# Kernel optimization log

Hardware: AMD Instinct MI355X
Metric: run time of the kernel (lower is better)

Reference implementation:

```python
import jax, jax.numpy as jnp
import numpy as np

B, N = 4, 2048
VD, CD = 256, 64
H = 4
INNER = VD  # inner_ratio = 1
D = INNER // H  # head_dim = 64
EPS = 1e-5
RMS_EPS = 1e-6


def layer_norm(x, g, b):
    m = jnp.mean(x, axis=-1, keepdims=True)
    v = jnp.mean((x - m) ** 2, axis=-1, keepdims=True)
    return (x - m) * jax.lax.rsqrt(v + EPS) * g + b


def rms_norm(x, s):
    ms = jnp.mean(x * x, axis=-1, keepdims=True)
    return x * jax.lax.rsqrt(ms + RMS_EPS) * s


def split_heads(x):  # (b, n, h*d) -> (b, h, n, d)
    b, n, _ = x.shape
    return x.reshape(b, n, H, D).transpose(0, 2, 1, 3)


def setup_inputs() -> dict:
    key = jax.random.key(0)
    ks = jax.random.split(key, 10)
    w = lambda k, shp: jax.random.normal(k, shp, dtype=jnp.float32) * 0.02
    return {
        "V": jax.random.normal(ks[0], (B, N, VD), dtype=jnp.float32),
        "C": jax.random.normal(ks[1], (B, N, CD), dtype=jnp.float32),
        "vn_g": jnp.ones((VD,), jnp.float32), "vn_b": jnp.zeros((VD,), jnp.float32),
        "cn_g": jnp.ones((CD,), jnp.float32), "cn_b": jnp.zeros((CD,), jnp.float32),
        "W_vqk": w(ks[2], (VD, 2 * INNER)), "b_vqk": jnp.zeros((2 * INNER,), jnp.float32),
        "rms_v": jnp.ones((2 * INNER,), jnp.float32),
        "W_cqk": w(ks[3], (CD, 2 * INNER)), "b_cqk": jnp.zeros((2 * INNER,), jnp.float32),
        "rms_c": jnp.ones((2 * INNER,), jnp.float32),
        "W_vv": w(ks[4], (VD, INNER)), "b_vv": jnp.zeros((INNER,), jnp.float32),
        "W_cv": w(ks[5], (CD, INNER)), "b_cv": jnp.zeros((INNER,), jnp.float32),
        "W_ov": w(ks[6], (INNER, VD)), "b_ov": jnp.zeros((VD,), jnp.float32),
        "W_oc": w(ks[7], (INNER, CD)), "b_oc": jnp.zeros((CD,), jnp.float32),
    }


def reference(V, C, vn_g, vn_b, cn_g, cn_b, W_vqk, b_vqk, rms_v, W_cqk, b_cqk, rms_c,
              W_vv, b_vv, W_cv, b_cv, W_ov, b_ov, W_oc, b_oc):
    Vn = layer_norm(V, vn_g, vn_b)
    Cn = layer_norm(C, cn_g, cn_b)
    qkv = rms_norm(Vn @ W_vqk + b_vqk, rms_v)
    qkc = rms_norm(Cn @ W_cqk + b_cqk, rms_c)
    qv, kv = jnp.split(qkv, 2, axis=-1)
    qc, kc = jnp.split(qkc, 2, axis=-1)
    vv = Vn @ W_vv + b_vv
    vc = Cn @ W_cv + b_cv
    qv, kv, vv, qc, kc, vc = map(split_heads, (qv, kv, vv, qc, kc, vc))
    # shared attention map: softmax((QvKv^T + QcKc^T)/sqrt(d))
    scores = (jnp.einsum("bhnd,bhmd->bhnm", qv, kv)
              + jnp.einsum("bhnd,bhmd->bhnm", qc, kc)) / np.sqrt(D).astype(np.float32)
    attn = jax.nn.softmax(scores, axis=-1)
    out_v = jnp.einsum("bhnm,bhmd->bhnd", attn, vv).transpose(0, 2, 1, 3).reshape(B, N, INNER)
    out_c = jnp.einsum("bhnm,bhmd->bhnd", attn, vc).transpose(0, 2, 1, 3).reshape(B, N, INNER)
    return out_v @ W_ov + b_ov, out_c @ W_oc + b_oc
```

## Files before the change

### kernel.cpp

```cpp
#include <hip/hip_runtime.h>

typedef unsigned short u16;
typedef unsigned int   u32;
typedef short s16x8 __attribute__((ext_vector_type(8)));
typedef float f32x4 __attribute__((ext_vector_type(4)));

#define WS_STATSV 0
#define WS_STATSC 65536
#define WS_WT_VQK 131072
#define WS_WT_CQK 393216
#define WS_WT_VV  458752
#define WS_WT_CV  589824
#define WS_WT_OV  622592
#define WS_WT_OC  753664
#define WS_Q      786432
#define WS_K      9175040
#define WS_VT     17563648
#define WS_OV     25952256
#define WS_OC     30146560

__device__ __forceinline__ float bf2f(u16 h){
  union { u32 u; float f; } x; x.u = ((u32)h) << 16; return x.f;
}
__device__ __forceinline__ u16 f2bf(float f){
  union { float f; u32 u; } x; x.f = f;
  u32 u = x.u; u += 0x7fffu + ((u >> 16) & 1u);
  return (u16)(u >> 16);
}
__device__ __forceinline__ f32x4 mfma16(s16x8 a, s16x8 b, f32x4 c){
  return __builtin_amdgcn_mfma_f32_16x16x32_bf16(a, b, c, 0, 0, 0);
}

__global__ __launch_bounds__(256) void k_prep(const float* V, const float* C,
    const float* vng, const float* vnb, const float* cng, const float* cnb,
    const float* Wvqk, const float* Wcqk, const float* Wvv, const float* Wcv,
    const float* Wov, const float* Woc, char* ws){
  int bid = blockIdx.x;
  if (bid < 4096){
    int wid = threadIdx.x >> 6, lane = threadIdx.x & 63;
    if (bid < 2048){
      int row = bid*4 + wid;
      const float4* p = (const float4*)(V + row*256);
      float4 v = p[lane];
      float s = v.x+v.y+v.z+v.w, s2 = v.x*v.x+v.y*v.y+v.z*v.z+v.w*v.w;
      for (int d=1; d<64; d<<=1){ s += __shfl_xor(s,d); s2 += __shfl_xor(s2,d); }
      float m = s*(1.0f/256.0f); float var = s2*(1.0f/256.0f) - m*m; if (var < 0.f) var = 0.f;
      float rstd = rsqrtf(var + 1e-5f), nb = -m*rstd;
      float4 gg = ((const float4*)vng)[lane];
      float4 bb = ((const float4*)vnb)[lane];
      ushort4 pk;
      pk.x = f2bf(fmaf(fmaf(v.x, rstd, nb), gg.x, bb.x));
      pk.y = f2bf(fmaf(fmaf(v.y, rstd, nb), gg.y, bb.y));
      pk.z = f2bf(fmaf(fmaf(v.z, rstd, nb), gg.z, bb.z));
      pk.w = f2bf(fmaf(fmaf(v.w, rstd, nb), gg.w, bb.w));
      *(ushort4*)((u16*)(ws + WS_OV) + row*256 + lane*4) = pk;
    } else {
      int row = (bid-2048)*4 + wid;
      float x = C[row*64 + lane];
      float s = x, s2 = x*x;
      for (int d=1; d<64; d<<=1){ s += __shfl_xor(s,d); s2 += __shfl_xor(s2,d); }
      float m = s*(1.0f/64.0f); float var = s2*(1.0f/64.0f) - m*m; if (var < 0.f) var = 0.f;
      float rstd = rsqrtf(var + 1e-5f);
      float xn = fmaf(fmaf(x, rstd, -m*rstd), cng[lane], cnb[lane]);
      ((u16*)(ws + WS_OC))[row*64 + lane] = f2bf(xn);
    }
  } else {
    int tb = bid - 4096;
    const float* src; u16* dst; int K, N, rel;
    if      (tb <  64){ src=Wvqk; dst=(u16*)(ws+WS_WT_VQK); K=256; N=512; rel=tb;     }
    else if (tb <  80){ src=Wcqk; dst=(u16*)(ws+WS_WT_CQK); K=64;  N=512; rel=tb-64;  }
    else if (tb < 112){ src=Wvv;  dst=(u16*)(ws+WS_WT_VV);  K=256; N=256; rel=tb-80;  }
    else if (tb < 120){ src=Wcv;  dst=(u16*)(ws+WS_WT_CV);  K=64;  N=256; rel=tb-112; }
    else if (tb < 152){ src=Wov;  dst=(u16*)(ws+WS_WT_OV);  K=256; N=256; rel=tb-120; }
    else              { src=Woc;  dst=(u16*)(ws+WS_WT_OC);  K=256; N=64;  rel=tb-152; }
    int e = rel*2048 + threadIdx.x*8;
    int k = e / N, n0 = e % N;
    float4 t0 = *(const float4*)(src + e);
    float4 t1 = *(const float4*)(src + e + 4);
    dst[(n0+0)*K + k] = f2bf(t0.x);
    dst[(n0+1)*K + k] = f2bf(t0.y);
    dst[(n0+2)*K + k] = f2bf(t0.z);
    dst[(n0+3)*K + k] = f2bf(t0.w);
    dst[(n0+4)*K + k] = f2bf(t1.x);
    dst[(n0+5)*K + k] = f2bf(t1.y);
    dst[(n0+6)*K + k] = f2bf(t1.z);
    dst[(n0+7)*K + k] = f2bf(t1.w);
  }
}

__global__ __launch_bounds__(256) void k_proj(const float* bvqk, const float* bcqk,
    const float* rmsv, const float* rmsc, const float* bvv, const float* bcv, char* ws){
  __shared__ float ssl[4][4][16];
  __shared__ u16 qst[2][2304];
  __shared__ u16 kst[2][2048];
  int bid = blockIdx.x;
  int tid = threadIdx.x, lane = tid & 63, w = tid >> 6;
  int c = lane & 15, q = lane >> 4;

  if (bid < 256){
    bool csd = bid >= 128;
    int rb = (bid & 127) * 64;
    const u16* An    = (const u16*)(ws + (csd ? WS_OC : WS_OV));
    int K            = csd ? 64 : 256;
    const u16* Wt    = (const u16*)(ws + (csd ? WS_WT_CQK : WS_WT_VQK));
    const float* bias= csd ? bcqk : bvqk;
    const float* rms = csd ? rmsc : rmsv;
    int dOff         = csd ? 64 : 0;

    int j0 = w * 128;

    f32x4 acc[4][8];
    #pragma unroll
    for (int s=0;s<4;s++)
      #pragma unroll
      for (int f=0; f<8; f++){ f32x4 z = {0.f,0.f,0.f,0.f}; acc[s][f] = z; }

    int nkc = K >> 5;
    for (int kc=0; kc<nkc; kc++){
      int k0 = kc*32 + q*8;
      s16x8 af[4];
      #pragma unroll
      for (int s=0;s<4;s++) af[s] = *(const s16x8*)(An + (rb + s*16 + c)*K + k0);
      #pragma unroll
      for (int f=0; f<8; f++){
        s16x8 bfr = *(const s16x8*)(Wt + (j0 + f*16 + c)*K + k0);
        #pragma unroll
        for (int s=0;s<4;s++) acc[s][f] = mfma16(af[s], bfr, acc[s][f]);
      }
    }

    float ss[4][4];
    #pragma unroll
    for (int s=0;s<4;s++)
      #pragma unroll
      for (int i=0;i<4;i++) ss[s][i] = 0.f;
    float rsv[8];
    #pragma unroll
    for (int f=0; f<8; f++){
      int j = j0 + f*16 + c;
      float bsv = bias[j]; rsv[f] = rms[j];
      #pragma unroll
      for (int s=0;s<4;s++)
        #pragma unroll
        for (int i=0;i<4;i++){ acc[s][f][i] += bsv; ss[s][i] += acc[s][f][i]*acc[s][f][i]; }
    }
    #pragma unroll
    for (int d=1; d<16; d<<=1){
      #pragma unroll
      for (int s=0;s<4;s++)
        #pragma unroll
        for (int i=0;i<4;i++) ss[s][i] += __shfl_xor(ss[s][i], d);
    }
    if (c == 0){
      #pragma unroll
      for (int s=0;s<4;s++)
        #pragma unroll
        for (int i=0;i<4;i++) ssl[w][s][q*4 + i] = ss[s][i];
    }
    __syncthreads();
    float rmsr[4][4];
    #pragma unroll
    for (int s=0;s<4;s++)
      #pragma unroll
      for (int i=0;i<4;i++){
        int rl = q*4 + i;
        float tot = ssl[0][s][rl] + ssl[1][s][rl] + ssl[2][s][rl] + ssl[3][s][rl];
        rmsr[s][i] = rsqrtf(tot * (1.0f/512.0f) + 1e-6f);
      }
    int b_ = rb >> 11;
    if (w < 2){
      u16* qs_ = &qst[w][0];
      u16* dstb = (u16*)(ws + WS_Q);
      const float qscale = 0.125f*1.44269504f;
      int headbase = w*2;
      #pragma unroll
      for (int s=0;s<4;s++){
        int n0g = (rb + s*16) & 2047;
        #pragma unroll
        for (int f=0; f<8; f++){
          int hl = f >> 2, dloc = (f&3)*16 + c;
          #pragma unroll
          for (int i=0;i<4;i++)
            qs_[hl*1152 + (q*4+i)*72 + dloc] = f2bf(acc[s][f][i]*rmsr[s][i]*rsv[f]*qscale);
        }
        #pragma unroll
        for (int it=0; it<4; it++){
          int hl = it>>1, token = (it&1)*8 + (lane>>3), dloc = (lane&7)*8;
          uint4 v = *(uint4*)&qs_[hl*1152 + token*72 + dloc];
          *(uint4*)(dstb + ((b_*4 + headbase + hl)*2048 + n0g + token)*128 + dOff + dloc) = v;
        }
      }
    } else {
      u16* ks_ = &kst[w-2][0];
      u16* kfb = (u16*)(ws + WS_K);
      int headbase = (w-2)*2;
      int kcOff = dOff >> 5;
      #pragma unroll
      for (int s=0;s<4;s++){
        int n0g = (rb + s*16) & 2047;
        int t = n0g >> 5, fK = (n0g >> 4) & 1;
        #pragma unroll
        for (int f=0; f<8; f++){
          int hl = f >> 2, ddl = (f&3)*16 + c;
          int kcl = ddl >> 5, qK = (ddl >> 3) & 3, eK = ddl & 7;
          #pragma unroll
          for (int i=0;i<4;i++)
            ks_[hl*1024 + kcl*512 + qK*128 + (q*4+i)*8 + eK]
              = f2bf(acc[s][f][i]*rmsr[s][i]*rsv[f]);
        }
        #pragma unroll
        for (int it=0; it<4; it++){
          int hl = it>>1, kcl = it&1;
          uint4 v = *(uint4*)&ks_[hl*1024 + kcl*512 + lane*8];
          *(uint4*)(kfb + (b_*4 + headbase + hl)*262144 + t*4096
                        + (fK*4 + kcOff + kcl)*512 + lane*8) = v;
        }
      }
    }
  } else {
    int vb2 = bid - 256;
    bool csd = vb2 >= 128;
    int rb = (vb2 & 127) * 64;
    const u16* An    = (const u16*)(ws + (csd ? WS_OC : WS_OV));
    int K            = csd ? 64 : 256;
    const u16* Wt    = (const u16*)(ws + (csd ? WS_WT_CV : WS_WT_VV));
    const float* bias= csd ? bcv : bvv;
    int dOff         = csd ? 64 : 0;

    int cgp = w & 1, sl2 = w >> 1;
    int r0 = rb + sl2*32;
    int j0 = cgp * 128;

    f32x4 acc[2][8];
    #pragma unroll
    for (int s=0;s<2;s++)
      #pragma unroll
      for (int f=0; f<8; f++){ f32x4 z = {0.f,0.f,0.f,0.f}; acc[s][f] = z; }

    int nkc = K >> 5;
    for (int kc=0; kc<nkc; kc++){
      int k0 = kc*32 + q*8;
      s16x8 af0 = *(const s16x8*)(An + (r0 + c)*K + k0);
      s16x8 af1 = *(const s16x8*)(An + (r0 + 16 + c)*K + k0);
      #pragma unroll
      for (int f=0; f<8; f++){
        s16x8 bfr = *(const s16x8*)(Wt + (j0 + f*16 + c)*K + k0);
        acc[0][f] = mfma16(af0, bfr, acc[0][f]);
        acc[1][f] = mfma16(af1, bfr, acc[1][f]);
      }
    }
    u16* vfb = (u16*)(ws + WS_VT);
    #pragma unroll
    for (int s=0;s<2;s++){
      int r = r0 + s*16 + q*4;
      int b_ = r >> 11, n = r & 2047;
      int t = n >> 5, m = n & 31;
      int qV = (m < 16) ? (m >> 2) : ((m >> 2) - 4);
      int e0 = (m < 16) ? 0 : 4;
      #pragma unroll
      for (int f=0; f<8; f++){
        int j = j0 + f*16 + c;
        float bv_ = bias[j];
        int head = j >> 6, dd = (j & 63) + dOff;
        int f8 = dd >> 4, cV = dd & 15;
        ushort4 pk;
        pk.x = f2bf(acc[s][f][0] + bv_); pk.y = f2bf(acc[s][f][1] + bv_);
        pk.z = f2bf(acc[s][f][2] + bv_); pk.w = f2bf(acc[s][f][3] + bv_);
        *(ushort4*)(vfb + (b_*4 + head)*262144 + t*4096 + f8*512 + (qV*16 + cV)*8 + e0) = pk;
      }
    }
  }
}

__global__ __launch_bounds__(256, 2) void k_attn(char* ws){
  const u16* Qw = (const u16*)(ws + WS_Q);
  const u16* KF = (const u16*)(ws + WS_K);
  const u16* VF = (const u16*)(ws + WS_VT);
  u16* Ov = (u16*)(ws + WS_OV);
  u16* Oc = (u16*)(ws + WS_OC);
  __shared__ float mg[2][64][67];

  int bh = blockIdx.x & 15, qb = blockIdx.x >> 4;
  int tid = threadIdx.x, lane = tid & 63, w = tid >> 6;
  int c = lane & 15, q = lane >> 4;
  int g = w & 1, h = w >> 1;
  int qr0 = qb*64 + g*32;

  s16x8 qf[2][4];
  #pragma unroll
  for (int s=0;s<2;s++)
    #pragma unroll
    for (int kc=0;kc<4;kc++)
      qf[s][kc] = *(const s16x8*)(Qw + (bh*2048 + qr0 + s*16 + c)*128 + kc*32 + q*8);

  const u16* kb = KF + bh*262144 + h*131072 + lane*8;
  const u16* vb = VF + bh*262144 + h*131072 + lane*8;

  f32x4 o[2][8];
  float lsum[2] = {0.f, 0.f};
  #pragma unroll
  for (int s=0;s<2;s++)
    #pragma unroll
    for (int f8=0;f8<8;f8++){ f32x4 z = {0.f,0.f,0.f,0.f}; o[s][f8] = z; }

  s16x8 kA[2][4], vA[8], kB[2][4], vB[8];

  auto loadT = [&](s16x8 (&kf)[2][4], s16x8 (&vf)[8], int tt){
    const u16* kt = kb + tt*4096;
    const u16* vt = vb + tt*4096;
    #pragma unroll
    for (int f=0;f<2;f++)
      #pragma unroll
      for (int kc=0;kc<4;kc++)
        kf[f][kc] = *(const s16x8*)(kt + (f*4+kc)*512);
    #pragma unroll
    for (int f8=0;f8<8;f8++)
      vf[f8] = *(const s16x8*)(vt + f8*512);
  };

  auto comp = [&](const s16x8 (&kf)[2][4], const s16x8 (&vf)[8]){
    f32x4 sfr[2][2];
    #pragma unroll
    for (int s=0;s<2;s++)
      #pragma unroll
      for (int f=0;f<2;f++){ f32x4 z = {0.f,0.f,0.f,0.f}; sfr[s][f] = z; }
    #pragma unroll
    for (int s=0;s<2;s++)
      #pragma unroll
      for (int f=0;f<2;f++)
        #pragma unroll
        for (int kc=0;kc<4;kc++)
          sfr[s][f] = mfma16(kf[f][kc], qf[s][kc], sfr[s][f]);

    #pragma unroll
    for (int s=0;s<2;s++){
      float p0 = exp2f(sfr[s][0][0]), p1 = exp2f(sfr[s][0][1]);
      float p2 = exp2f(sfr[s][0][2]), p3 = exp2f(sfr[s][0][3]);
      float p4 = exp2f(sfr[s][1][0]), p5 = exp2f(sfr[s][1][1]);
      float p6 = exp2f(sfr[s][1][2]), p7 = exp2f(sfr[s][1][3]);
      lsum[s] += ((p0+p1)+(p2+p3)) + ((p4+p5)+(p6+p7));
      union { u32 u[4]; s16x8 v; } pa;
      pa.u[0] = (u32)f2bf(p0) | ((u32)f2bf(p1) << 16);
      pa.u[1] = (u32)f2bf(p2) | ((u32)f2bf(p3) << 16);
      pa.u[2] = (u32)f2bf(p4) | ((u32)f2bf(p5) << 16);
      pa.u[3] = (u32)f2bf(p6) | ((u32)f2bf(p7) << 16);
      #pragma unroll
      for (int f8=0;f8<8;f8++)
        o[s][f8] = mfma16(pa.v, vf[f8], o[s][f8]);
    }
  };

  loadT(kA, vA, 0);
  for (int tt=0; tt<32; tt+=2){
    loadT(kB, vB, tt+1);
    comp(kA, vA);
    if (tt+2 < 32) loadT(kA, vA, tt+2);
    comp(kB, vB);
  }

  __syncthreads();
  if (h == 1){
    float* d = &mg[g][lane][0];
    #pragma unroll
    for (int s=0;s<2;s++)
      #pragma unroll
      for (int f8=0;f8<8;f8++)
        #pragma unroll
        for (int i=0;i<4;i++) d[(s*8+f8)*4 + i] = o[s][f8][i];
    d[64] = lsum[0]; d[65] = lsum[1];
  }
  __syncthreads();
  if (h == 0){
    float* d = &mg[g][lane][0];
    #pragma unroll
    for (int s=0;s<2;s++)
      #pragma unroll
      for (int f8=0;f8<8;f8++)
        #pragma unroll
        for (int i=0;i<4;i++) o[s][f8][i] += d[(s*8+f8)*4 + i];
    lsum[0] += d[64]; lsum[1] += d[65];

    #pragma unroll
    for (int s=0;s<2;s++){
      lsum[s] += __shfl_xor(lsum[s], 16);
      lsum[s] += __shfl_xor(lsum[s], 32);
    }

    int b_ = bh >> 2, hh = bh & 3;
    #pragma unroll
    for (int s=0;s<2;s++){
      float inv[4];
      #pragma unroll
      for (int i=0;i<4;i++) inv[i] = 1.0f/__shfl(lsum[s], q*4 + i);
      #pragma unroll
      for (int f8=0;f8<8;f8++){
        int col = f8*16 + c;
        u16* dst = (col < 64) ? Ov : Oc;
        int ddim = col & 63;
        #pragma unroll
        for (int i=0;i<4;i++){
          int n = qr0 + s*16 + q*4 + i;
          dst[(b_*2048 + n)*256 + hh*64 + ddim] = f2bf(o[s][f8][i]*inv[i]);
        }
      }
    }
  }
}

__global__ __launch_bounds__(256) void k_out(const u16* Av, const u16* Wtv, const float* bv,
                                             const u16* Ac, const u16* Wtc, const float* bc,
                                             float* out){
  int bid = blockIdx.x;
  int tid = threadIdx.x, lane = tid & 63, w = tid >> 6;
  int c = lane & 15, q = lane >> 4;
  if (bid < 128){
    int rb = bid * 64;
    int j0 = w * 64;
    f32x4 acc[4][4];
    #pragma unroll
    for (int s=0;s<4;s++)
      #pragma unroll
      for (int f=0; f<4; f++){ f32x4 z = {0.f,0.f,0.f,0.f}; acc[s][f] = z; }
    for (int kc=0; kc<8; kc++){
      int k0 = kc*32 + q*8;
      s16x8 af[4];
      #pragma unroll
      for (int s=0;s<4;s++) af[s] = *(const s16x8*)(Av + (rb + s*16 + c)*256 + k0);
      #pragma unroll
      for (int f=0; f<4; f++){
        s16x8 bfr = *(const s16x8*)(Wtv + (j0 + f*16 + c)*256 + k0);
        #pragma unroll
        for (int s=0;s<4;s++) acc[s][f] = mfma16(af[s], bfr, acc[s][f]);
      }
    }
    #pragma unroll
    for (int f=0; f<4; f++){
      int j = j0 + f*16 + c;
      float bb = bv[j];
      #pragma unroll
      for (int s=0;s<4;s++)
        #pragma unroll
        for (int i=0;i<4;i++)
          out[(rb + s*16 + q*4 + i)*256 + j] = acc[s][f][i] + bb;
    }
  } else {
    int rb = (bid - 128) * 128;
    int r0 = rb + w*32;
    f32x4 acc[2][4];
    #pragma unroll
    for (int s=0;s<2;s++)
      #pragma unroll
      for (int f=0; f<4; f++){ f32x4 z = {0.f,0.f,0.f,0.f}; acc[s][f] = z; }
    for (int kc=0; kc<8; kc++){
      int k0 = kc*32 + q*8;
      s16x8 af0 = *(const s16x8*)(Ac + (r0 + c)*256 + k0);
      s16x8 af1 = *(const s16x8*)(Ac + (r0 + 16 + c)*256 + k0);
      #pragma unroll
      for (int f=0; f<4; f++){
        s16x8 bfr = *(const s16x8*)(Wtc + (f*16 + c)*256 + k0);
        acc[0][f] = mfma16(af0, bfr, acc[0][f]);
        acc[1][f] = mfma16(af1, bfr, acc[1][f]);
      }
    }
    float* oc = out + 2097152;
    #pragma unroll
    for (int f=0; f<4; f++){
      int j = f*16 + c;
      float bb = bc[j];
      #pragma unroll
      for (int s=0;s<2;s++)
        #pragma unroll
        for (int i=0;i<4;i++)
          oc[(r0 + s*16 + q*4 + i)*64 + j] = acc[s][f][i] + bb;
    }
  }
}

extern "C" void kernel_launch(void* const* d_in, const int* in_sizes, int n_in,
                              void* d_out, int out_size, void* d_ws, size_t ws_size,
                              hipStream_t stream){
  (void)in_sizes; (void)n_in; (void)out_size; (void)ws_size;
  const float* V    = (const float*)d_in[0];
  const float* C    = (const float*)d_in[1];
  const float* vng  = (const float*)d_in[2];
  const float* vnb  = (const float*)d_in[3];
  const float* cng  = (const float*)d_in[4];
  const float* cnb  = (const float*)d_in[5];
  const float* Wvqk = (const float*)d_in[6];
  const float* bvqk = (const float*)d_in[7];
  const float* rmsv = (const float*)d_in[8];
  const float* Wcqk = (const float*)d_in[9];
  const float* bcqk = (const float*)d_in[10];
  const float* rmsc = (const float*)d_in[11];
  const float* Wvv  = (const float*)d_in[12];
  const float* bvv  = (const float*)d_in[13];
  const float* Wcv  = (const float*)d_in[14];
  const float* bcv  = (const float*)d_in[15];
  const float* Wov  = (const float*)d_in[16];
  const float* bov  = (const float*)d_in[17];
  const float* Woc  = (const float*)d_in[18];
  const float* boc  = (const float*)d_in[19];
  char* ws = (char*)d_ws;
  float* out = (float*)d_out;

  k_prep<<<4256, 256, 0, stream>>>(V, C, vng, vnb, cng, cnb,
                                   Wvqk, Wcqk, Wvv, Wcv, Wov, Woc, ws);
  k_proj<<<512, 256, 0, stream>>>(bvqk, bcqk, rmsv, rmsc, bvv, bcv, ws);
  k_attn<<<512, 256, 0, stream>>>(ws);
  k_out<<<192, 256, 0, stream>>>((const u16*)(ws + WS_OV), (const u16*)(ws + WS_WT_OV), bov,
                                 (const u16*)(ws + WS_OC), (const u16*)(ws + WS_WT_OC), boc,
                                 out);
}
```

Baseline: 187.8 us.

## Fuse layer norms into projection kernel via shared-memory staging

Result: slower. 191.8 us (+2.1%).

```diff
diff --git a/kernel.cpp b/kernel.cpp
--- a/kernel.cpp
+++ b/kernel.cpp
@@ -31,76 +31,81 @@
   return __builtin_amdgcn_mfma_f32_16x16x32_bf16(a, b, c, 0, 0, 0);
 }
 
-__global__ __launch_bounds__(256) void k_prep(const float* V, const float* C,
+__global__ __launch_bounds__(256) void k_prep(const float* Wvqk, const float* Wcqk,
+    const float* Wvv, const float* Wcv, const float* Wov, const float* Woc, char* ws){
+  int tb = blockIdx.x;
+  const float* src; u16* dst; int K, N, rel;
+  if      (tb <  64){ src=Wvqk; dst=(u16*)(ws+WS_WT_VQK); K=256; N=512; rel=tb;     }
+  else if (tb <  80){ src=Wcqk; dst=(u16*)(ws+WS_WT_CQK); K=64;  N=512; rel=tb-64;  }
+  else if (tb < 112){ src=Wvv;  dst=(u16*)(ws+WS_WT_VV);  K=256; N=256; rel=tb-80;  }
+  else if (tb < 120){ src=Wcv;  dst=(u16*)(ws+WS_WT_CV);  K=64;  N=256; rel=tb-112; }
+  else if (tb < 152){ src=Wov;  dst=(u16*)(ws+WS_WT_OV);  K=256; N=256; rel=tb-120; }
+  else              { src=Woc;  dst=(u16*)(ws+WS_WT_OC);  K=256; N=64;  rel=tb-152; }
+  int e = rel*2048 + threadIdx.x*8;
+  int k = e / N, n0 = e % N;
+  float4 t0 = *(const float4*)(src + e);
+  float4 t1 = *(const float4*)(src + e + 4);
+  dst[(n0+0)*K + k] = f2bf(t0.x);
+  dst[(n0+1)*K + k] = f2bf(t0.y);
+  dst[(n0+2)*K + k] = f2bf(t0.z);
+  dst[(n0+3)*K + k] = f2bf(t0.w);
+  dst[(n0+4)*K + k] = f2bf(t1.x);
+  dst[(n0+5)*K + k] = f2bf(t1.y);
+  dst[(n0+6)*K + k] = f2bf(t1.z);
+  dst[(n0+7)*K + k] = f2bf(t1.w);
+}
+
+__global__ __launch_bounds__(256) void k_proj(const float* V, const float* C,
     const float* vng, const float* vnb, const float* cng, const float* cnb,
-    const float* Wvqk, const float* Wcqk, const float* Wvv, const float* Wcv,
-    const float* Wov, const float* Woc, char* ws){
+    const float* bvqk, const float* bcqk, const float* rmsv, const float* rmsc,
+    const float* bvv, const float* bcv, char* ws){
+  __shared__ float ssl[4][4][16];
+  __shared__ u16 qst[2][2304];
+  __shared__ u16 kst[2][2048];
+  __shared__ u16 Asm[16896];
   int bid = blockIdx.x;
-  if (bid < 4096){
-    int wid = threadIdx.x >> 6, lane = threadIdx.x & 63;
-    if (bid < 2048){
-      int row = bid*4 + wid;
-      const float4* p = (const float4*)(V + row*256);
-      float4 v = p[lane];
+  int tid = threadIdx.x, lane = tid & 63, w = tid >> 6;
+  int c = lane & 15, q = lane >> 4;
+
+  bool csd = (bid >> 7) & 1;
+  int rb = (bid & 127) * 64;
+  int astr = csd ? 72 : 264;
+
+  if (!csd){
+    float4 gg = ((const float4*)vng)[lane];
+    float4 bb = ((const float4*)vnb)[lane];
+    #pragma unroll 4
+    for (int rr=0; rr<16; rr++){
+      int row = rb + w*16 + rr;
+      float4 v = ((const float4*)(V + row*256))[lane];
       float s = v.x+v.y+v.z+v.w, s2 = v.x*v.x+v.y*v.y+v.z*v.z+v.w*v.w;
       for (int d=1; d<64; d<<=1){ s += __shfl_xor(s,d); s2 += __shfl_xor(s2,d); }
       float m = s*(1.0f/256.0f); float var = s2*(1.0f/256.0f) - m*m; if (var < 0.f) var = 0.f;
       float rstd = rsqrtf(var + 1e-5f), nb = -m*rstd;
-      float4 gg = ((const float4*)vng)[lane];
-      float4 bb = ((const float4*)vnb)[lane];
       ushort4 pk;
       pk.x = f2bf(fmaf(fmaf(v.x, rstd, nb), gg.x, bb.x));
       pk.y = f2bf(fmaf(fmaf(v.y, rstd, nb), gg.y, bb.y));
       pk.z = f2bf(fmaf(fmaf(v.z, rstd, nb), gg.z, bb.z));
       pk.w = f2bf(fmaf(fmaf(v.w, rstd, nb), gg.w, bb.w));
-      *(ushort4*)((u16*)(ws + WS_OV) + row*256 + lane*4) = pk;
-    } else {
-      int row = (bid-2048)*4 + wid;
+      *(ushort4*)&Asm[(w*16+rr)*264 + lane*4] = pk;
+    }
+  } else {
+    float cg = cng[lane], cb = cnb[lane];
+    #pragma unroll 4
+    for (int rr=0; rr<16; rr++){
+      int row = rb + w*16 + rr;
       float x = C[row*64 + lane];
       float s = x, s2 = x*x;
       for (int d=1; d<64; d<<=1){ s += __shfl_xor(s,d); s2 += __shfl_xor(s2,d); }
       float m = s*(1.0f/64.0f); float var = s2*(1.0f/64.0f) - m*m; if (var < 0.f) var = 0.f;
       float rstd = rsqrtf(var + 1e-5f);
-      float xn = fmaf(fmaf(x, rstd, -m*rstd), cng[lane], cnb[lane]);
-      ((u16*)(ws + WS_OC))[row*64 + lane] = f2bf(xn);
-    }
-  } else {
-    int tb = bid - 4096;
-    const float* src; u16* dst; int K, N, rel;
-    if      (tb <  64){ src=Wvqk; dst=(u16*)(ws+WS_WT_VQK); K=256; N=512; rel=tb;     }
-    else if (tb <  80){ src=Wcqk; dst=(u16*)(ws+WS_WT_CQK); K=64;  N=512; rel=tb-64;  }
-    else if (tb < 112){ src=Wvv;  dst=(u16*)(ws+WS_WT_VV);  K=256; N=256; rel=tb-80;  }
-    else if (tb < 120){ src=Wcv;  dst=(u16*)(ws+WS_WT_CV);  K=64;  N=256; rel=tb-112; }
-    else if (tb < 152){ src=Wov;  dst=(u16*)(ws+WS_WT_OV);  K=256; N=256; rel=tb-120; }
-    else              { src=Woc;  dst=(u16*)(ws+WS_WT_OC);  K=256; N=64;  rel=tb-152; }
-    int e = rel*2048 + threadIdx.x*8;
-    int k = e / N, n0 = e % N;
-    float4 t0 = *(const float4*)(src + e);
-    float4 t1 = *(const float4*)(src + e + 4);
-    dst[(n0+0)*K + k] = f2bf(t0.x);
-    dst[(n0+1)*K + k] = f2bf(t0.y);
-    dst[(n0+2)*K + k] = f2bf(t0.z);
-    dst[(n0+3)*K + k] = f2bf(t0.w);
-    dst[(n0+4)*K + k] = f2bf(t1.x);
-    dst[(n0+5)*K + k] = f2bf(t1.y);
-    dst[(n0+6)*K + k] = f2bf(t1.z);
-    dst[(n0+7)*K + k] = f2bf(t1.w);
+      float xn = fmaf(fmaf(x, rstd, -m*rstd), cg, cb);
+      Asm[(w*16+rr)*72 + lane] = f2bf(xn);
+    }
   }
-}
-
-__global__ __launch_bounds__(256) void k_proj(const float* bvqk, const float* bcqk,
-    const float* rmsv, const float* rmsc, const float* bvv, const float* bcv, char* ws){
-  __shared__ float ssl[4][4][16];
-  __shared__ u16 qst[2][2304];
-  __shared__ u16 kst[2][2048];
-  int bid = blockIdx.x;
-  int tid = threadIdx.x, lane = tid & 63, w = tid >> 6;
-  int c = lane & 15, q = lane >> 4;
+  __syncthreads();
 
   if (bid < 256){
-    bool csd = bid >= 128;
-    int rb = (bid & 127) * 64;
-    const u16* An    = (const u16*)(ws + (csd ? WS_OC : WS_OV));
     int K            = csd ? 64 : 256;
     const u16* Wt    = (const u16*)(ws + (csd ? WS_WT_CQK : WS_WT_VQK));
     const float* bias= csd ? bcqk : bvqk;
@@ -120,7 +125,7 @@
       int k0 = kc*32 + q*8;
       s16x8 af[4];
       #pragma unroll
-      for (int s=0;s<4;s++) af[s] = *(const s16x8*)(An + (rb + s*16 + c)*K + k0);
+      for (int s=0;s<4;s++) af[s] = *(const s16x8*)&Asm[(s*16 + c)*astr + k0];
       #pragma unroll
       for (int f=0; f<8; f++){
         s16x8 bfr = *(const s16x8*)(Wt + (j0 + f*16 + c)*K + k0);
@@ -218,17 +223,12 @@
       }
     }
   } else {
-    int vb2 = bid - 256;
-    bool csd = vb2 >= 128;
-    int rb = (vb2 & 127) * 64;
-    const u16* An    = (const u16*)(ws + (csd ? WS_OC : WS_OV));
     int K            = csd ? 64 : 256;
     const u16* Wt    = (const u16*)(ws + (csd ? WS_WT_CV : WS_WT_VV));
     const float* bias= csd ? bcv : bvv;
     int dOff         = csd ? 64 : 0;
 
     int cgp = w & 1, sl2 = w >> 1;
-    int r0 = rb + sl2*32;
     int j0 = cgp * 128;
 
     f32x4 acc[2][8];
@@ -240,8 +240,8 @@
     int nkc = K >> 5;
     for (int kc=0; kc<nkc; kc++){
       int k0 = kc*32 + q*8;
-      s16x8 af0 = *(const s16x8*)(An + (r0 + c)*K + k0);
-      s16x8 af1 = *(const s16x8*)(An + (r0 + 16 + c)*K + k0);
+      s16x8 af0 = *(const s16x8*)&Asm[(sl2*32 + c)*astr + k0];
+      s16x8 af1 = *(const s16x8*)&Asm[(sl2*32 + 16 + c)*astr + k0];
       #pragma unroll
       for (int f=0; f<8; f++){
         s16x8 bfr = *(const s16x8*)(Wt + (j0 + f*16 + c)*K + k0);
@@ -252,7 +252,7 @@
     u16* vfb = (u16*)(ws + WS_VT);
     #pragma unroll
     for (int s=0;s<2;s++){
-      int r = r0 + s*16 + q*4;
+      int r = rb + sl2*32 + s*16 + q*4;
       int b_ = r >> 11, n = r & 2047;
       int t = n >> 5, m = n & 31;
       int qV = (m < 16) ? (m >> 2) : ((m >> 2) - 4);
@@ -503,9 +503,9 @@
   char* ws = (char*)d_ws;
   float* out = (float*)d_out;
 
-  k_prep<<<4256, 256, 0, stream>>>(V, C, vng, vnb, cng, cnb,
-                                   Wvqk, Wcqk, Wvv, Wcv, Wov, Woc, ws);
-  k_proj<<<512, 256, 0, stream>>>(bvqk, bcqk, rmsv, rmsc, bvv, bcv, ws);
+  k_prep<<<160, 256, 0, stream>>>(Wvqk, Wcqk, Wvv, Wcv, Wov, Woc, ws);
+  k_proj<<<512, 256, 0, stream>>>(V, C, vng, vnb, cng, cnb,
+                                  bvqk, bcqk, rmsv, rmsc, bvv, bcv, ws);
   k_attn<<<512, 256, 0, stream>>>(ws);
   k_out<<<192, 256, 0, stream>>>((const u16*)(ws + WS_OV), (const u16*)(ws + WS_WT_OV), bov,
                                  (const u16*)(ws + WS_OC), (const u16*)(ws + WS_WT_OC), boc,
```

## Split attention KV range four ways per block and double grid size

Applied to the files above, without the earlier changes.

Result: no change. 191.0 us (+1.7%).

```diff
diff --git a/kernel.cpp b/kernel.cpp
--- a/kernel.cpp
+++ b/kernel.cpp
@@ -281,10 +281,9 @@
   __shared__ float mg[2][64][67];
 
   int bh = blockIdx.x & 15, qb = blockIdx.x >> 4;
-  int tid = threadIdx.x, lane = tid & 63, w = tid >> 6;
+  int tid = threadIdx.x, lane = tid & 63, h = tid >> 6;
   int c = lane & 15, q = lane >> 4;
-  int g = w & 1, h = w >> 1;
-  int qr0 = qb*64 + g*32;
+  int qr0 = qb*32;
 
   s16x8 qf[2][4];
   #pragma unroll
@@ -293,8 +292,8 @@
     for (int kc=0;kc<4;kc++)
       qf[s][kc] = *(const s16x8*)(Qw + (bh*2048 + qr0 + s*16 + c)*128 + kc*32 + q*8);
 
-  const u16* kb = KF + bh*262144 + h*131072 + lane*8;
-  const u16* vb = VF + bh*262144 + h*131072 + lane*8;
+  const u16* kb = KF + bh*262144 + h*65536 + lane*8;
+  const u16* vb = VF + bh*262144 + h*65536 + lane*8;
 
   f32x4 o[2][8];
   float lsum[2] = {0.f, 0.f};
@@ -351,16 +350,16 @@
   };
 
   loadT(kA, vA, 0);
-  for (int tt=0; tt<32; tt+=2){
+  for (int tt=0; tt<16; tt+=2){
     loadT(kB, vB, tt+1);
     comp(kA, vA);
-    if (tt+2 < 32) loadT(kA, vA, tt+2);
+    if (tt+2 < 16) loadT(kA, vA, tt+2);
     comp(kB, vB);
   }
 
   __syncthreads();
-  if (h == 1){
-    float* d = &mg[g][lane][0];
+  if (h == 1 || h == 3){
+    float* d = &mg[h>>1][lane][0];
     #pragma unroll
     for (int s=0;s<2;s++)
       #pragma unroll
@@ -370,8 +369,30 @@
     d[64] = lsum[0]; d[65] = lsum[1];
   }
   __syncthreads();
+  if (h == 0 || h == 2){
+    float* d = &mg[h>>1][lane][0];
+    #pragma unroll
+    for (int s=0;s<2;s++)
+      #pragma unroll
+      for (int f8=0;f8<8;f8++)
+        #pragma unroll
+        for (int i=0;i<4;i++) o[s][f8][i] += d[(s*8+f8)*4 + i];
+    lsum[0] += d[64]; lsum[1] += d[65];
+  }
+  __syncthreads();
+  if (h == 2){
+    float* d = &mg[0][lane][0];
+    #pragma unroll
+    for (int s=0;s<2;s++)
+      #pragma unroll
+      for (int f8=0;f8<8;f8++)
+        #pragma unroll
+        for (int i=0;i<4;i++) d[(s*8+f8)*4 + i] = o[s][f8][i];
+    d[64] = lsum[0]; d[65] = lsum[1];
+  }
+  __syncthreads();
   if (h == 0){
-    float* d = &mg[g][lane][0];
+    float* d = &mg[0][lane][0];
     #pragma unroll
     for (int s=0;s<2;s++)
       #pragma unroll
@@ -506,7 +527,7 @@
   k_prep<<<4256, 256, 0, stream>>>(V, C, vng, vnb, cng, cnb,
                                    Wvqk, Wcqk, Wvv, Wcv, Wov, Woc, ws);
   k_proj<<<512, 256, 0, stream>>>(bvqk, bcqk, rmsv, rmsc, bvv, bcv, ws);
-  k_attn<<<512, 256, 0, stream>>>(ws);
+  k_attn<<<1024, 256, 0, stream>>>(ws);
   k_out<<<192, 256, 0, stream>>>((const u16*)(ws + WS_OV), (const u16*)(ws + WS_WT_OV), bov,
                                  (const u16*)(ws + WS_OC), (const u16*)(ws + WS_WT_OC), boc,
                                  out);
```
